# Kernel optimization log

Measured on AMD Instinct MI355X. Metric: run time of the kernel, lower is better.

Reference implementation:

```python
import jax, jax.numpy as jnp
import numpy as np

B, C, H, W = 2, 256, 32, 32
PK, CK = 256, 256


def setup_inputs() -> dict:
    key = jax.random.key(0)
    ks = jax.random.split(key, 9)
    s = 1.0 / np.sqrt(C)
    return {
        'x': jax.random.normal(ks[0], (B, C, H, W), jnp.float32),
        'primary_indices': jax.random.randint(ks[1], (B, PK), 0, B * H * W),
        'compare_indices': jax.random.randint(ks[2], (B, CK), 0, B * H * W),
        'pre_w': jax.random.uniform(ks[3], (3, C, C), jnp.float32, -s, s),
        'pre_b': jax.random.uniform(ks[4], (3, C), jnp.float32, -s, s),
        'post_w': jax.random.uniform(ks[5], (2, C, C), jnp.float32, -s, s),
        'post_b': jax.random.uniform(ks[6], (2, C), jnp.float32, -s, s),
        'post_out_w': jax.random.uniform(ks[7], (2, C), jnp.float32, -s, s),
        'post_out_b': jax.random.uniform(ks[8], (2,), jnp.float32, -s, s),
    }


def reference(x, primary_indices, compare_indices, pre_w, pre_b,
              post_w, post_b, post_out_w, post_out_b):
    # pre_compare: stack of 1x1 convs (c->c->c->c), ReLU between layers
    h = x
    for i in range(3):
        h = jnp.einsum('bchw,oc->bohw', h, pre_w[i]) + pre_b[i][None, :, None, None]
        if i < 2:
            h = jax.nn.relu(h)
    bs, c, hh, ww = h.shape
    # flatten to [bs*h*w, c] node features (matches torch transpose+reshape)
    flat = h.reshape(bs, c, hh * ww).transpose(0, 2, 1).reshape(bs * hh * ww, c)
    # gather primary / compare node features with global flat indices
    xp = flat[primary_indices.reshape(-1)].reshape(bs, -1, c).transpose(0, 2, 1)  # [b,c,pk]
    xc = flat[compare_indices.reshape(-1)].reshape(bs, -1, c).transpose(0, 2, 1)  # [b,c,ck]
    # broadcast pairwise squared difference -> [b,c,pk,ck]
    xx = (xp[:, :, :, None] - xc[:, :, None, :]) ** 2
    # post_compare: 1x1 conv stack c->c->c->2, ReLU between layers
    g = xx
    for i in range(2):
        g = jax.nn.relu(jnp.einsum('bcpq,oc->bopq', g, post_w[i]) + post_b[i][None, :, None, None])
    out = jnp.einsum('bcpq,oc->bopq', g, post_out_w) + post_out_b[None, :, None, None]
    return out  # [b, 2, pk, ck]
```

## Files before the change

### kernel.cpp

```cpp
#include <hip/hip_runtime.h>

typedef unsigned short u16;
typedef short bf16x8 __attribute__((ext_vector_type(8)));
typedef float f32x4 __attribute__((ext_vector_type(4)));
typedef u16 u16x4 __attribute__((ext_vector_type(4)));

__device__ __forceinline__ float b2f(u16 h) {
  unsigned u = ((unsigned)h) << 16;
  return __builtin_bit_cast(float, u);
}
__device__ __forceinline__ u16 f2b(float f) {
  unsigned u = __builtin_bit_cast(unsigned, f);
  u = u + 0x7fffu + ((u >> 16) & 1u);
  return (u16)(u >> 16);
}

#if defined(__has_builtin)
#if __has_builtin(__builtin_amdgcn_cvt_pk_bf16_f32)
#define HAVE_CVT_PK_BF16 1
#endif
#endif

__device__ __forceinline__ unsigned f2b_pk(float a, float b) {
#ifdef HAVE_CVT_PK_BF16
  auto v = __builtin_amdgcn_cvt_pk_bf16_f32(a, b);
  unsigned r;
  __builtin_memcpy(&r, &v, 4);
  return r;
#else
  return (unsigned)f2b(a) | (((unsigned)f2b(b)) << 16);
#endif
}
__device__ __forceinline__ bf16x8 pack8(const float* v) {
  union { unsigned u[4]; bf16x8 o; } r;
  r.u[0] = f2b_pk(v[0], v[1]);
  r.u[1] = f2b_pk(v[2], v[3]);
  r.u[2] = f2b_pk(v[4], v[5]);
  r.u[3] = f2b_pk(v[6], v[7]);
  return r.o;
}
__device__ __forceinline__ u16x4 pack4(float a, float b, float c, float d) {
  union { unsigned u[2]; u16x4 o; } r;
  r.u[0] = f2b_pk(a, b);
  r.u[1] = f2b_pk(c, d);
  return r.o;
}
__device__ __forceinline__ void gld_lds16(const void* g, void* l) {
  __builtin_amdgcn_global_load_lds(
      (__attribute__((address_space(1))) void*)(g),
      (__attribute__((address_space(3))) void*)(l), 16, 0, 0);
}

__global__ void dense_edge_prep(const float* __restrict__ x,
                                const float* __restrict__ pre_w,
                                const float* __restrict__ post_w,
                                u16* __restrict__ wb, u16* __restrict__ xt) {
  const int blk = blockIdx.x;
  const int t = threadIdx.x;
  if (blk < 160) {
    const int id = blk * 256 + t;
    const int layer = id >> 13;
    const int sid = id & 8191;
    const int m = sid >> 5;
    const int s8 = sid & 31;
    const float* src = (layer < 2) ? (post_w + layer * 65536)
                                   : (pre_w + (layer - 2) * 65536);
    u16* dst = wb + layer * 65536;
    f32x4 a = *(const f32x4*)(src + m * 256 + s8 * 8);
    f32x4 c = *(const f32x4*)(src + m * 256 + s8 * 8 + 4);
    float tmp[8] = {a[0], a[1], a[2], a[3], c[0], c[1], c[2], c[3]};
    *(bf16x8*)(dst + (s8 * 256 + m) * 8) = pack8(tmp);
  } else {
    __shared__ float tile[32 * 65];
    const int xb = blk - 160;
    const int b = xb >> 7;
    const int ct = (xb >> 4) & 7;
    const int ht = xb & 15;
    const int c0 = ct * 32, hw0 = ht * 64;
#pragma unroll
    for (int rep = 0; rep < 8; rep++) {
      const int idx = rep * 256 + t;
      const int cl = idx >> 6, hl = idx & 63;
      tile[cl * 65 + hl] = x[(b * 256 + c0 + cl) * 1024 + hw0 + hl];
    }
    __syncthreads();
    const int hl = t >> 2, c8 = t & 3;
    float tmp[8];
#pragma unroll
    for (int i = 0; i < 8; i++) tmp[i] = tile[(c8 * 8 + i) * 65 + hl];
    *(bf16x8*)(xt + (b * 1024 + hw0 + hl) * 256 + c0 + c8 * 8) = pack8(tmp);
  }
}

__global__ __launch_bounds__(256, 2) void dense_edge_pre(
    const u16* __restrict__ xt, const u16* __restrict__ wpre,
    const float* __restrict__ preb, u16* __restrict__ flat) {
  __shared__ u16 feat[2][4096];
  const int t = threadIdx.x;
  const int wv = t >> 6, ln = t & 63;
  const int nb = blockIdx.x * 16;
  const int q4 = ln >> 4, r15 = ln & 15;

#pragma unroll
  for (int i = 0; i < 2; i++) {
    const int slot = wv * 128 + i * 64 + ln;
    const int s8 = slot >> 4, nl = slot & 15;
    gld_lds16(xt + (nb + nl) * 256 + s8 * 8, &feat[0][slot * 8]);
  }
  __syncthreads();

#pragma unroll
  for (int l = 0; l < 3; l++) {
    const u16* wl = wpre + l * 65536;
    f32x4 acc[4];
    f32x4 zero = {0.f, 0.f, 0.f, 0.f};
#pragma unroll
    for (int mt = 0; mt < 4; mt++) acc[mt] = zero;
#pragma unroll
    for (int s = 0; s < 8; s++) {
      bf16x8 bv = *(const bf16x8*)(&feat[l & 1][((s * 4 + q4) * 16 + r15) * 8]);
#pragma unroll
      for (int mt = 0; mt < 4; mt++) {
        bf16x8 av = *(const bf16x8*)(wl + ((s * 4 + q4) * 256 + wv * 64 + mt * 16 + r15) * 8);
        acc[mt] = __builtin_amdgcn_mfma_f32_16x16x32_bf16(av, bv, acc[mt], 0, 0, 0);
      }
    }
    if (l < 2) {
#pragma unroll
      for (int mt = 0; mt < 4; mt++) {
        const int o = wv * 64 + mt * 16 + q4 * 4;
        f32x4 bb = *(const f32x4*)(preb + l * 256 + o);
        *(u16x4*)(&feat[(l + 1) & 1][((o >> 3) * 16 + r15) * 8 + (o & 7)]) =
            pack4(fmaxf(acc[mt][0] + bb[0], 0.f), fmaxf(acc[mt][1] + bb[1], 0.f),
                  fmaxf(acc[mt][2] + bb[2], 0.f), fmaxf(acc[mt][3] + bb[3], 0.f));
      }
      __syncthreads();
    } else {
#pragma unroll
      for (int mt = 0; mt < 4; mt++) {
        const int o = wv * 64 + mt * 16 + q4 * 4;
        f32x4 bb = *(const f32x4*)(preb + 512 + o);
        *(u16x4*)(flat + (nb + r15) * 256 + o) =
            pack4(acc[mt][0] + bb[0], acc[mt][1] + bb[1],
                  acc[mt][2] + bb[2], acc[mt][3] + bb[3]);
      }
    }
  }
}

__global__ __launch_bounds__(256, 2) void dense_edge_main(
    const u16* __restrict__ flat, const int* __restrict__ pidx,
    const int* __restrict__ cidx, const u16* __restrict__ w1s,
    const u16* __restrict__ w2s, const float* __restrict__ b1,
    const float* __restrict__ b2, const float* __restrict__ w3,
    const float* __restrict__ b3, float* __restrict__ out) {
  __shared__ u16 xxbuf[16384];
  __shared__ u16 t1buf[16384];
  __shared__ float pbuf[4][2][64];

  const int t = threadIdx.x;
  const int wv = t >> 6;
  const int ln = t & 63;
  const int q4 = ln >> 4, r15 = ln & 15;
  const int blk = blockIdx.x;
  const int b = blk >> 10;
  const int pt = (blk >> 5) & 31;
  const int qt = blk & 31;
  const int p0 = pt * 8, q0 = qt * 8;

  bf16x8 af_w[4][8];
#pragma unroll
  for (int s = 0; s < 8; s++)
#pragma unroll
    for (int mt = 0; mt < 4; mt++)
      af_w[mt][s] = *(const bf16x8*)(w1s + ((s * 4 + q4) * 256 + wv * 64 + mt * 16 + r15) * 8);

  {
    const int pn = pidx[b * 256 + p0 + (ln >> 3)];
    const int qn = cidx[b * 256 + q0 + (ln & 7)];
    const u16* prow = flat + pn * 256 + wv * 64;
    const u16* qrow = flat + qn * 256 + wv * 64;
#pragma unroll
    for (int i = 0; i < 8; i++) {
      bf16x8 av = *(const bf16x8*)(prow + i * 8);
      bf16x8 bv = *(const bf16x8*)(qrow + i * 8);
      float d[8];
#pragma unroll
      for (int jj = 0; jj < 8; jj++) {
        float dv = b2f((u16)av[jj]) - b2f((u16)bv[jj]);
        d[jj] = dv * dv;
      }
      *(bf16x8*)(xxbuf + ((wv * 8 + i) * 64 + ln) * 8) = pack8(d);
    }
  }
  __syncthreads();

  f32x4 acc[4][4];
  {
    f32x4 zero = {0.f, 0.f, 0.f, 0.f};
#pragma unroll
    for (int mt = 0; mt < 4; mt++)
#pragma unroll
      for (int nt = 0; nt < 4; nt++) acc[mt][nt] = zero;
  }
#pragma unroll
  for (int s = 0; s < 8; s++) {
    bf16x8 bfr[4];
#pragma unroll
    for (int nt = 0; nt < 4; nt++)
      bfr[nt] = *(const bf16x8*)(xxbuf + ((s * 4 + q4) * 64 + nt * 16 + r15) * 8);
#pragma unroll
    for (int mt = 0; mt < 4; mt++)
#pragma unroll
      for (int nt = 0; nt < 4; nt++)
        acc[mt][nt] = __builtin_amdgcn_mfma_f32_16x16x32_bf16(af_w[mt][s], bfr[nt], acc[mt][nt], 0, 0, 0);
  }

#pragma unroll
  for (int mt = 0; mt < 4; mt++) {
    const int o = wv * 64 + mt * 16 + q4 * 4;
    f32x4 bb = *(const f32x4*)(b1 + o);
#pragma unroll
    for (int nt = 0; nt < 4; nt++) {
      const int nn = nt * 16 + r15;
      *(u16x4*)(t1buf + ((o >> 3) * 64 + nn) * 8 + (o & 7)) =
          pack4(fmaxf(acc[mt][nt][0] + bb[0], 0.f),
                fmaxf(acc[mt][nt][1] + bb[1], 0.f),
                fmaxf(acc[mt][nt][2] + bb[2], 0.f),
                fmaxf(acc[mt][nt][3] + bb[3], 0.f));
      acc[mt][nt][0] = 0.f; acc[mt][nt][1] = 0.f;
      acc[mt][nt][2] = 0.f; acc[mt][nt][3] = 0.f;
    }
  }
#pragma unroll
  for (int s = 0; s < 8; s++)
#pragma unroll
    for (int mt = 0; mt < 4; mt++)
      af_w[mt][s] = *(const bf16x8*)(w2s + ((s * 4 + q4) * 256 + wv * 64 + mt * 16 + r15) * 8);
  __syncthreads();

#pragma unroll
  for (int s = 0; s < 8; s++) {
    bf16x8 bfr[4];
#pragma unroll
    for (int nt = 0; nt < 4; nt++)
      bfr[nt] = *(const bf16x8*)(t1buf + ((s * 4 + q4) * 64 + nt * 16 + r15) * 8);
#pragma unroll
    for (int mt = 0; mt < 4; mt++)
#pragma unroll
      for (int nt = 0; nt < 4; nt++)
        acc[mt][nt] = __builtin_amdgcn_mfma_f32_16x16x32_bf16(af_w[mt][s], bfr[nt], acc[mt][nt], 0, 0, 0);
  }

  {
    float part[2][4] = {{0.f, 0.f, 0.f, 0.f}, {0.f, 0.f, 0.f, 0.f}};
#pragma unroll
    for (int mt = 0; mt < 4; mt++) {
      const int o = wv * 64 + mt * 16 + q4 * 4;
      f32x4 bb = *(const f32x4*)(b2 + o);
      f32x4 w3a = *(const f32x4*)(w3 + o);
      f32x4 w3b = *(const f32x4*)(w3 + 256 + o);
#pragma unroll
      for (int nt = 0; nt < 4; nt++) {
#pragma unroll
        for (int r = 0; r < 4; r++) {
          float v = fmaxf(acc[mt][nt][r] + bb[r], 0.f);
          part[0][nt] += v * w3a[r];
          part[1][nt] += v * w3b[r];
        }
      }
    }
#pragma unroll
    for (int o3 = 0; o3 < 2; o3++)
#pragma unroll
      for (int nt = 0; nt < 4; nt++) {
        part[o3][nt] += __shfl_xor(part[o3][nt], 16, 64);
        part[o3][nt] += __shfl_xor(part[o3][nt], 32, 64);
      }
    if (q4 == 0) {
#pragma unroll
      for (int o3 = 0; o3 < 2; o3++)
#pragma unroll
        for (int nt = 0; nt < 4; nt++)
          pbuf[wv][o3][nt * 16 + r15] = part[o3][nt];
    }
  }
  __syncthreads();

  if (t < 128) {
    const int o3 = t >> 6;
    const int n = t & 63;
    float v = b3[o3] + pbuf[0][o3][n] + pbuf[1][o3][n] + pbuf[2][o3][n] + pbuf[3][o3][n];
    out[((b * 2 + o3) * 256 + p0 + (n >> 3)) * 256 + q0 + (n & 7)] = v;
  }
}

extern "C" void kernel_launch(void* const* d_in, const int* in_sizes, int n_in,
                              void* d_out, int out_size, void* d_ws, size_t ws_size,
                              hipStream_t stream) {
  (void)in_sizes; (void)n_in; (void)out_size; (void)ws_size;
  const float* x          = (const float*)d_in[0];
  const int*   pidx       = (const int*)d_in[1];
  const int*   cidx       = (const int*)d_in[2];
  const float* pre_w      = (const float*)d_in[3];
  const float* pre_b      = (const float*)d_in[4];
  const float* post_w     = (const float*)d_in[5];
  const float* post_b     = (const float*)d_in[6];
  const float* post_out_w = (const float*)d_in[7];
  const float* post_out_b = (const float*)d_in[8];
  float* out = (float*)d_out;

  u16* ws   = (u16*)d_ws;
  u16* w1s  = ws;
  u16* w2s  = ws + 65536;
  u16* wpre = ws + 131072;
  u16* xt   = ws + 327680;
  u16* flat = ws + 851968;

  dense_edge_prep<<<416, 256, 0, stream>>>(x, pre_w, post_w, ws, xt);
  dense_edge_pre<<<128, 256, 0, stream>>>(xt, wpre, pre_b, flat);
  dense_edge_main<<<2048, 256, 0, stream>>>(flat, pidx, cidx, w1s, w2s,
                                            post_b, post_b + 256,
                                            post_out_w, post_out_b, out);
}
```

Before: 129.3 us.

## Fuse prep, pre-conv and edge MLP into one persistent kernel with grid barrier

Merges the three launches into a single 512-block kernel. Blocks 0-127 do the pre-conv stack, reading x directly and transposing it in shared memory, and convert pre weights to bf16 on the fly. Blocks 128-191 convert the post weights. An atomic-counter grid barrier then separates this from the edge MLP phase, where each block processes four output tiles. The goal is to remove launch overhead and the xt/wpre intermediate buffers, at the cost of a spin barrier that relies on all 512 blocks being co-resident, plus redundant per-tile weight fragment loads.

```diff
diff --git a/kernel.cpp b/kernel.cpp
--- a/kernel.cpp
+++ b/kernel.cpp
@@ -4,6 +4,8 @@
 typedef short bf16x8 __attribute__((ext_vector_type(8)));
 typedef float f32x4 __attribute__((ext_vector_type(4)));
 typedef u16 u16x4 __attribute__((ext_vector_type(4)));
+
+#define GRID_BLOCKS 512
 
 __device__ __forceinline__ float b2f(u16 h) {
   unsigned u = ((unsigned)h) << 16;
@@ -45,253 +47,251 @@
   r.u[1] = f2b_pk(c, d);
   return r.o;
 }
-__device__ __forceinline__ void gld_lds16(const void* g, void* l) {
-  __builtin_amdgcn_global_load_lds(
-      (__attribute__((address_space(1))) void*)(g),
-      (__attribute__((address_space(3))) void*)(l), 16, 0, 0);
-}
-
-__global__ void dense_edge_prep(const float* __restrict__ x,
-                                const float* __restrict__ pre_w,
-                                const float* __restrict__ post_w,
-                                u16* __restrict__ wb, u16* __restrict__ xt) {
+
+__global__ __launch_bounds__(256, 2) void dense_edge_fused(
+    const float* __restrict__ x, const int* __restrict__ pidx,
+    const int* __restrict__ cidx, const float* __restrict__ pre_w,
+    const float* __restrict__ preb, const float* __restrict__ post_w,
+    const float* __restrict__ postb, const float* __restrict__ w3,
+    const float* __restrict__ b3, float* __restrict__ out,
+    int* __restrict__ ctr, u16* __restrict__ w1s, u16* __restrict__ w2s,
+    u16* __restrict__ flat) {
+  __shared__ union {
+    struct { float xtile[256 * 20]; u16 feat[2][4096]; } pre;
+    struct { u16 xxbuf[16384]; u16 t1buf[16384]; float pbuf[4][2][64]; } mn;
+  } sm;
+
   const int blk = blockIdx.x;
   const int t = threadIdx.x;
-  if (blk < 160) {
-    const int id = blk * 256 + t;
+  const int wv = t >> 6, ln = t & 63;
+  const int q4 = ln >> 4, r15 = ln & 15;
+
+  if (blk >= 128 && blk < 192) {
+    const int id = (blk - 128) * 256 + t;
     const int layer = id >> 13;
     const int sid = id & 8191;
     const int m = sid >> 5;
     const int s8 = sid & 31;
-    const float* src = (layer < 2) ? (post_w + layer * 65536)
-                                   : (pre_w + (layer - 2) * 65536);
-    u16* dst = wb + layer * 65536;
-    f32x4 a = *(const f32x4*)(src + m * 256 + s8 * 8);
-    f32x4 c = *(const f32x4*)(src + m * 256 + s8 * 8 + 4);
+    const float* src = post_w + layer * 65536 + m * 256 + s8 * 8;
+    u16* dst = layer ? w2s : w1s;
+    f32x4 a = *(const f32x4*)(src);
+    f32x4 c = *(const f32x4*)(src + 4);
     float tmp[8] = {a[0], a[1], a[2], a[3], c[0], c[1], c[2], c[3]};
     *(bf16x8*)(dst + (s8 * 256 + m) * 8) = pack8(tmp);
-  } else {
-    __shared__ float tile[32 * 65];
-    const int xb = blk - 160;
-    const int b = xb >> 7;
-    const int ct = (xb >> 4) & 7;
-    const int ht = xb & 15;
-    const int c0 = ct * 32, hw0 = ht * 64;
-#pragma unroll
-    for (int rep = 0; rep < 8; rep++) {
-      const int idx = rep * 256 + t;
-      const int cl = idx >> 6, hl = idx & 63;
-      tile[cl * 65 + hl] = x[(b * 256 + c0 + cl) * 1024 + hw0 + hl];
-    }
-    __syncthreads();
-    const int hl = t >> 2, c8 = t & 3;
-    float tmp[8];
-#pragma unroll
-    for (int i = 0; i < 8; i++) tmp[i] = tile[(c8 * 8 + i) * 65 + hl];
-    *(bf16x8*)(xt + (b * 1024 + hw0 + hl) * 256 + c0 + c8 * 8) = pack8(tmp);
+  } else if (blk < 128) {
+    const int nb = blk * 16;
+    const int b0 = nb >> 10;
+    const int hw0 = nb & 1023;
+    {
+      const float* src = x + (b0 * 256 + t) * 1024 + hw0;
+      f32x4 v0 = *(const f32x4*)(src);
+      f32x4 v1 = *(const f32x4*)(src + 4);
+      f32x4 v2 = *(const f32x4*)(src + 8);
+      f32x4 v3 = *(const f32x4*)(src + 12);
+      *(f32x4*)&sm.pre.xtile[t * 20 + 0] = v0;
+      *(f32x4*)&sm.pre.xtile[t * 20 + 4] = v1;
+      *(f32x4*)&sm.pre.xtile[t * 20 + 8] = v2;
+      *(f32x4*)&sm.pre.xtile[t * 20 + 12] = v3;
+    }
+    __syncthreads();
+#pragma unroll
+    for (int rep = 0; rep < 2; rep++) {
+      const int id = rep * 256 + t;
+      const int n = id & 15, s8 = id >> 4;
+      float tmp[8];
+#pragma unroll
+      for (int j = 0; j < 8; j++) tmp[j] = sm.pre.xtile[(s8 * 8 + j) * 20 + n];
+      *(bf16x8*)(&sm.pre.feat[0][(s8 * 16 + n) * 8]) = pack8(tmp);
+    }
+    __syncthreads();
+#pragma unroll
+    for (int l = 0; l < 3; l++) {
+      const float* wl = pre_w + l * 65536;
+      f32x4 acc[4];
+      f32x4 zero = {0.f, 0.f, 0.f, 0.f};
+#pragma unroll
+      for (int mt = 0; mt < 4; mt++) acc[mt] = zero;
+#pragma unroll
+      for (int s = 0; s < 8; s++) {
+        bf16x8 bv = *(const bf16x8*)(&sm.pre.feat[l & 1][((s * 4 + q4) * 16 + r15) * 8]);
+#pragma unroll
+        for (int mt = 0; mt < 4; mt++) {
+          const float* wp = wl + (wv * 64 + mt * 16 + r15) * 256 + (s * 4 + q4) * 8;
+          f32x4 wa = *(const f32x4*)(wp);
+          f32x4 wc = *(const f32x4*)(wp + 4);
+          float tmp[8] = {wa[0], wa[1], wa[2], wa[3], wc[0], wc[1], wc[2], wc[3]};
+          bf16x8 av = pack8(tmp);
+          acc[mt] = __builtin_amdgcn_mfma_f32_16x16x32_bf16(av, bv, acc[mt], 0, 0, 0);
+        }
+      }
+      if (l < 2) {
+#pragma unroll
+        for (int mt = 0; mt < 4; mt++) {
+          const int o = wv * 64 + mt * 16 + q4 * 4;
+          f32x4 bb = *(const f32x4*)(preb + l * 256 + o);
+          *(u16x4*)(&sm.pre.feat[(l + 1) & 1][((o >> 3) * 16 + r15) * 8 + (o & 7)]) =
+              pack4(fmaxf(acc[mt][0] + bb[0], 0.f), fmaxf(acc[mt][1] + bb[1], 0.f),
+                    fmaxf(acc[mt][2] + bb[2], 0.f), fmaxf(acc[mt][3] + bb[3], 0.f));
+        }
+        __syncthreads();
+      } else {
+#pragma unroll
+        for (int mt = 0; mt < 4; mt++) {
+          const int o = wv * 64 + mt * 16 + q4 * 4;
+          f32x4 bb = *(const f32x4*)(preb + 512 + o);
+          *(u16x4*)(flat + (nb + r15) * 256 + o) =
+              pack4(acc[mt][0] + bb[0], acc[mt][1] + bb[1],
+                    acc[mt][2] + bb[2], acc[mt][3] + bb[3]);
+        }
+      }
+    }
   }
-}
-
-__global__ __launch_bounds__(256, 2) void dense_edge_pre(
-    const u16* __restrict__ xt, const u16* __restrict__ wpre,
-    const float* __restrict__ preb, u16* __restrict__ flat) {
-  __shared__ u16 feat[2][4096];
-  const int t = threadIdx.x;
-  const int wv = t >> 6, ln = t & 63;
-  const int nb = blockIdx.x * 16;
-  const int q4 = ln >> 4, r15 = ln & 15;
-
-#pragma unroll
-  for (int i = 0; i < 2; i++) {
-    const int slot = wv * 128 + i * 64 + ln;
-    const int s8 = slot >> 4, nl = slot & 15;
-    gld_lds16(xt + (nb + nl) * 256 + s8 * 8, &feat[0][slot * 8]);
+
+  __syncthreads();
+  if (t == 0) {
+    __threadfence();
+    atomicAdd(ctr, 1);
+    while (atomicAdd(ctr, 0) < GRID_BLOCKS) __builtin_amdgcn_s_sleep(8);
   }
   __syncthreads();
-
-#pragma unroll
-  for (int l = 0; l < 3; l++) {
-    const u16* wl = wpre + l * 65536;
-    f32x4 acc[4];
-    f32x4 zero = {0.f, 0.f, 0.f, 0.f};
-#pragma unroll
-    for (int mt = 0; mt < 4; mt++) acc[mt] = zero;
+  __threadfence();
+
+  const int tile0 = blk * 4;
+  const int b = tile0 >> 10;
+  const int pt = (tile0 >> 5) & 31;
+  const int p0 = pt * 8;
+  const int pn = pidx[b * 256 + p0 + (ln >> 3)];
+  const u16* prow = flat + pn * 256 + wv * 64;
+
+#pragma unroll 1
+  for (int i = 0; i < 4; i++) {
+    const int qt = (tile0 + i) & 31;
+    const int q0 = qt * 8;
+
+    bf16x8 af_w[4][8];
+#pragma unroll
+    for (int s = 0; s < 8; s++)
+#pragma unroll
+      for (int mt = 0; mt < 4; mt++)
+        af_w[mt][s] = *(const bf16x8*)(w1s + ((s * 4 + q4) * 256 + wv * 64 + mt * 16 + r15) * 8);
+
+    {
+      const int qn = cidx[b * 256 + q0 + (ln & 7)];
+      const u16* qrow = flat + qn * 256 + wv * 64;
+#pragma unroll
+      for (int ii = 0; ii < 8; ii++) {
+        bf16x8 av = *(const bf16x8*)(prow + ii * 8);
+        bf16x8 bv = *(const bf16x8*)(qrow + ii * 8);
+        float d[8];
+#pragma unroll
+        for (int jj = 0; jj < 8; jj++) {
+          float dv = b2f((u16)av[jj]) - b2f((u16)bv[jj]);
+          d[jj] = dv * dv;
+        }
+        *(bf16x8*)(sm.mn.xxbuf + ((wv * 8 + ii) * 64 + ln) * 8) = pack8(d);
+      }
+    }
+    __syncthreads();
+
+    f32x4 acc[4][4];
+    {
+      f32x4 zero = {0.f, 0.f, 0.f, 0.f};
+#pragma unroll
+      for (int mt = 0; mt < 4; mt++)
+#pragma unroll
+        for (int nt = 0; nt < 4; nt++) acc[mt][nt] = zero;
+    }
 #pragma unroll
     for (int s = 0; s < 8; s++) {
-      bf16x8 bv = *(const bf16x8*)(&feat[l & 1][((s * 4 + q4) * 16 + r15) * 8]);
-#pragma unroll
-      for (int mt = 0; mt < 4; mt++) {
-        bf16x8 av = *(const bf16x8*)(wl + ((s * 4 + q4) * 256 + wv * 64 + mt * 16 + r15) * 8);
-        acc[mt] = __builtin_amdgcn_mfma_f32_16x16x32_bf16(av, bv, acc[mt], 0, 0, 0);
-      }
-    }
-    if (l < 2) {
+      bf16x8 bfr[4];
+#pragma unroll
+      for (int nt = 0; nt < 4; nt++)
+        bfr[nt] = *(const bf16x8*)(sm.mn.xxbuf + ((s * 4 + q4) * 64 + nt * 16 + r15) * 8);
+#pragma unroll
+      for (int mt = 0; mt < 4; mt++)
+#pragma unroll
+        for (int nt = 0; nt < 4; nt++)
+          acc[mt][nt] = __builtin_amdgcn_mfma_f32_16x16x32_bf16(af_w[mt][s], bfr[nt], acc[mt][nt], 0, 0, 0);
+    }
+
+#pragma unroll
+    for (int mt = 0; mt < 4; mt++) {
+      const int o = wv * 64 + mt * 16 + q4 * 4;
+      f32x4 bb = *(const f32x4*)(postb + o);
+#pragma unroll
+      for (int nt = 0; nt < 4; nt++) {
+        const int nn = nt * 16 + r15;
+        *(u16x4*)(sm.mn.t1buf + ((o >> 3) * 64 + nn) * 8 + (o & 7)) =
+            pack4(fmaxf(acc[mt][nt][0] + bb[0], 0.f),
+                  fmaxf(acc[mt][nt][1] + bb[1], 0.f),
+                  fmaxf(acc[mt][nt][2] + bb[2], 0.f),
+                  fmaxf(acc[mt][nt][3] + bb[3], 0.f));
+        acc[mt][nt][0] = 0.f; acc[mt][nt][1] = 0.f;
+        acc[mt][nt][2] = 0.f; acc[mt][nt][3] = 0.f;
+      }
+    }
+#pragma unroll
+    for (int s = 0; s < 8; s++)
+#pragma unroll
+      for (int mt = 0; mt < 4; mt++)
+        af_w[mt][s] = *(const bf16x8*)(w2s + ((s * 4 + q4) * 256 + wv * 64 + mt * 16 + r15) * 8);
+    __syncthreads();
+
+#pragma unroll
+    for (int s = 0; s < 8; s++) {
+      bf16x8 bfr[4];
+#pragma unroll
+      for (int nt = 0; nt < 4; nt++)
+        bfr[nt] = *(const bf16x8*)(sm.mn.t1buf + ((s * 4 + q4) * 64 + nt * 16 + r15) * 8);
+#pragma unroll
+      for (int mt = 0; mt < 4; mt++)
+#pragma unroll
+        for (int nt = 0; nt < 4; nt++)
+          acc[mt][nt] = __builtin_amdgcn_mfma_f32_16x16x32_bf16(af_w[mt][s], bfr[nt], acc[mt][nt], 0, 0, 0);
+    }
+
+    {
+      float part[2][4] = {{0.f, 0.f, 0.f, 0.f}, {0.f, 0.f, 0.f, 0.f}};
 #pragma unroll
       for (int mt = 0; mt < 4; mt++) {
         const int o = wv * 64 + mt * 16 + q4 * 4;
-        f32x4 bb = *(const f32x4*)(preb + l * 256 + o);
-        *(u16x4*)(&feat[(l + 1) & 1][((o >> 3) * 16 + r15) * 8 + (o & 7)]) =
-            pack4(fmaxf(acc[mt][0] + bb[0], 0.f), fmaxf(acc[mt][1] + bb[1], 0.f),
-                  fmaxf(acc[mt][2] + bb[2], 0.f), fmaxf(acc[mt][3] + bb[3], 0.f));
-      }
-      __syncthreads();
-    } else {
-#pragma unroll
-      for (int mt = 0; mt < 4; mt++) {
-        const int o = wv * 64 + mt * 16 + q4 * 4;
-        f32x4 bb = *(const f32x4*)(preb + 512 + o);
-        *(u16x4*)(flat + (nb + r15) * 256 + o) =
-            pack4(acc[mt][0] + bb[0], acc[mt][1] + bb[1],
-                  acc[mt][2] + bb[2], acc[mt][3] + bb[3]);
-      }
-    }
-  }
-}
-
-__global__ __launch_bounds__(256, 2) void dense_edge_main(
-    const u16* __restrict__ flat, const int* __restrict__ pidx,
-    const int* __restrict__ cidx, const u16* __restrict__ w1s,
-    const u16* __restrict__ w2s, const float* __restrict__ b1,
-    const float* __restrict__ b2, const float* __restrict__ w3,
-    const float* __restrict__ b3, float* __restrict__ out) {
-  __shared__ u16 xxbuf[16384];
-  __shared__ u16 t1buf[16384];
-  __shared__ float pbuf[4][2][64];
-
-  const int t = threadIdx.x;
-  const int wv = t >> 6;
-  const int ln = t & 63;
-  const int q4 = ln >> 4, r15 = ln & 15;
-  const int blk = blockIdx.x;
-  const int b = blk >> 10;
-  const int pt = (blk >> 5) & 31;
-  const int qt = blk & 31;
-  const int p0 = pt * 8, q0 = qt * 8;
-
-  bf16x8 af_w[4][8];
-#pragma unroll
-  for (int s = 0; s < 8; s++)
-#pragma unroll
-    for (int mt = 0; mt < 4; mt++)
-      af_w[mt][s] = *(const bf16x8*)(w1s + ((s * 4 + q4) * 256 + wv * 64 + mt * 16 + r15) * 8);
-
-  {
-    const int pn = pidx[b * 256 + p0 + (ln >> 3)];
-    const int qn = cidx[b * 256 + q0 + (ln & 7)];
-    const u16* prow = flat + pn * 256 + wv * 64;
-    const u16* qrow = flat + qn * 256 + wv * 64;
-#pragma unroll
-    for (int i = 0; i < 8; i++) {
-      bf16x8 av = *(const bf16x8*)(prow + i * 8);
-      bf16x8 bv = *(const bf16x8*)(qrow + i * 8);
-      float d[8];
-#pragma unroll
-      for (int jj = 0; jj < 8; jj++) {
-        float dv = b2f((u16)av[jj]) - b2f((u16)bv[jj]);
-        d[jj] = dv * dv;
-      }
-      *(bf16x8*)(xxbuf + ((wv * 8 + i) * 64 + ln) * 8) = pack8(d);
-    }
-  }
-  __syncthreads();
-
-  f32x4 acc[4][4];
-  {
-    f32x4 zero = {0.f, 0.f, 0.f, 0.f};
-#pragma unroll
-    for (int mt = 0; mt < 4; mt++)
-#pragma unroll
-      for (int nt = 0; nt < 4; nt++) acc[mt][nt] = zero;
-  }
-#pragma unroll
-  for (int s = 0; s < 8; s++) {
-    bf16x8 bfr[4];
-#pragma unroll
-    for (int nt = 0; nt < 4; nt++)
-      bfr[nt] = *(const bf16x8*)(xxbuf + ((s * 4 + q4) * 64 + nt * 16 + r15) * 8);
-#pragma unroll
-    for (int mt = 0; mt < 4; mt++)
-#pragma unroll
-      for (int nt = 0; nt < 4; nt++)
-        acc[mt][nt] = __builtin_amdgcn_mfma_f32_16x16x32_bf16(af_w[mt][s], bfr[nt], acc[mt][nt], 0, 0, 0);
-  }
-
-#pragma unroll
-  for (int mt = 0; mt < 4; mt++) {
-    const int o = wv * 64 + mt * 16 + q4 * 4;
-    f32x4 bb = *(const f32x4*)(b1 + o);
-#pragma unroll
-    for (int nt = 0; nt < 4; nt++) {
-      const int nn = nt * 16 + r15;
-      *(u16x4*)(t1buf + ((o >> 3) * 64 + nn) * 8 + (o & 7)) =
-          pack4(fmaxf(acc[mt][nt][0] + bb[0], 0.f),
-                fmaxf(acc[mt][nt][1] + bb[1], 0.f),
-                fmaxf(acc[mt][nt][2] + bb[2], 0.f),
-                fmaxf(acc[mt][nt][3] + bb[3], 0.f));
-      acc[mt][nt][0] = 0.f; acc[mt][nt][1] = 0.f;
-      acc[mt][nt][2] = 0.f; acc[mt][nt][3] = 0.f;
-    }
-  }
-#pragma unroll
-  for (int s = 0; s < 8; s++)
-#pragma unroll
-    for (int mt = 0; mt < 4; mt++)
-      af_w[mt][s] = *(const bf16x8*)(w2s + ((s * 4 + q4) * 256 + wv * 64 + mt * 16 + r15) * 8);
-  __syncthreads();
-
-#pragma unroll
-  for (int s = 0; s < 8; s++) {
-    bf16x8 bfr[4];
-#pragma unroll
-    for (int nt = 0; nt < 4; nt++)
-      bfr[nt] = *(const bf16x8*)(t1buf + ((s * 4 + q4) * 64 + nt * 16 + r15) * 8);
-#pragma unroll
-    for (int mt = 0; mt < 4; mt++)
-#pragma unroll
-      for (int nt = 0; nt < 4; nt++)
-        acc[mt][nt] = __builtin_amdgcn_mfma_f32_16x16x32_bf16(af_w[mt][s], bfr[nt], acc[mt][nt], 0, 0, 0);
-  }
-
-  {
-    float part[2][4] = {{0.f, 0.f, 0.f, 0.f}, {0.f, 0.f, 0.f, 0.f}};
-#pragma unroll
-    for (int mt = 0; mt < 4; mt++) {
-      const int o = wv * 64 + mt * 16 + q4 * 4;
-      f32x4 bb = *(const f32x4*)(b2 + o);
-      f32x4 w3a = *(const f32x4*)(w3 + o);
-      f32x4 w3b = *(const f32x4*)(w3 + 256 + o);
-#pragma unroll
-      for (int nt = 0; nt < 4; nt++) {
-#pragma unroll
-        for (int r = 0; r < 4; r++) {
-          float v = fmaxf(acc[mt][nt][r] + bb[r], 0.f);
-          part[0][nt] += v * w3a[r];
-          part[1][nt] += v * w3b[r];
-        }
-      }
-    }
-#pragma unroll
-    for (int o3 = 0; o3 < 2; o3++)
-#pragma unroll
-      for (int nt = 0; nt < 4; nt++) {
-        part[o3][nt] += __shfl_xor(part[o3][nt], 16, 64);
-        part[o3][nt] += __shfl_xor(part[o3][nt], 32, 64);
-      }
-    if (q4 == 0) {
+        f32x4 bb = *(const f32x4*)(postb + 256 + o);
+        f32x4 w3a = *(const f32x4*)(w3 + o);
+        f32x4 w3b = *(const f32x4*)(w3 + 256 + o);
+#pragma unroll
+        for (int nt = 0; nt < 4; nt++) {
+#pragma unroll
+          for (int r = 0; r < 4; r++) {
+            float v = fmaxf(acc[mt][nt][r] + bb[r], 0.f);
+            part[0][nt] += v * w3a[r];
+            part[1][nt] += v * w3b[r];
+          }
+        }
+      }
 #pragma unroll
       for (int o3 = 0; o3 < 2; o3++)
 #pragma unroll
-        for (int nt = 0; nt < 4; nt++)
-          pbuf[wv][o3][nt * 16 + r15] = part[o3][nt];
-    }
-  }
-  __syncthreads();
-
-  if (t < 128) {
-    const int o3 = t >> 6;
-    const int n = t & 63;
-    float v = b3[o3] + pbuf[0][o3][n] + pbuf[1][o3][n] + pbuf[2][o3][n] + pbuf[3][o3][n];
-    out[((b * 2 + o3) * 256 + p0 + (n >> 3)) * 256 + q0 + (n & 7)] = v;
+        for (int nt = 0; nt < 4; nt++) {
+          part[o3][nt] += __shfl_xor(part[o3][nt], 16, 64);
+          part[o3][nt] += __shfl_xor(part[o3][nt], 32, 64);
+        }
+      if (q4 == 0) {
+#pragma unroll
+        for (int o3 = 0; o3 < 2; o3++)
+#pragma unroll
+          for (int nt = 0; nt < 4; nt++)
+            sm.mn.pbuf[wv][o3][nt * 16 + r15] = part[o3][nt];
+      }
+    }
+    __syncthreads();
+
+    if (t < 128) {
+      const int o3 = t >> 6;
+      const int n = t & 63;
+      float v = b3[o3] + sm.mn.pbuf[0][o3][n] + sm.mn.pbuf[1][o3][n] +
+                sm.mn.pbuf[2][o3][n] + sm.mn.pbuf[3][o3][n];
+      out[((b * 2 + o3) * 256 + p0 + (n >> 3)) * 256 + q0 + (n & 7)] = v;
+    }
   }
 }
 
@@ -310,16 +310,14 @@
   const float* post_out_b = (const float*)d_in[8];
   float* out = (float*)d_out;
 
-  u16* ws   = (u16*)d_ws;
-  u16* w1s  = ws;
-  u16* w2s  = ws + 65536;
-  u16* wpre = ws + 131072;
-  u16* xt   = ws + 327680;
-  u16* flat = ws + 851968;
-
-  dense_edge_prep<<<416, 256, 0, stream>>>(x, pre_w, post_w, ws, xt);
-  dense_edge_pre<<<128, 256, 0, stream>>>(xt, wpre, pre_b, flat);
-  dense_edge_main<<<2048, 256, 0, stream>>>(flat, pidx, cidx, w1s, w2s,
-                                            post_b, post_b + 256,
-                                            post_out_w, post_out_b, out);
-}
+  int* ctr  = (int*)d_ws;
+  u16* base = (u16*)d_ws;
+  u16* w1s  = base + 256;
+  u16* w2s  = base + 256 + 65536;
+  u16* flat = base + 256 + 131072;
+
+  hipMemsetAsync(d_ws, 0, 512, stream);
+  dense_edge_fused<<<GRID_BLOCKS, 256, 0, stream>>>(
+      x, pidx, cidx, pre_w, pre_b, post_w, post_b,
+      post_out_w, post_out_b, out, ctr, w1s, w2s, flat);
+}
```

Measured after the change: 296.0 us. 2.29x slower.
